# Kernel optimization log

Measured on AMD Instinct MI355X. Metric: run time of the kernel, lower is better.

The kernel has to match this reference:

```python
import jax, jax.numpy as jnp
import numpy as np

N = 30000        # nodes
E = 480000       # edges
IN = 256         # input feature dim
D = 32           # num_hidden per head
H = 4            # heads for layers 0,1
C = 47           # num_classes (final layer, 1 head)
NEG_SLOPE = 0.2


def setup_inputs() -> dict:
    key = jax.random.key(0)
    ks = jax.random.split(key, 16)
    def glorot(k, shape):
        fan = sum(shape)
        return jax.random.normal(k, shape, jnp.float32) * jnp.sqrt(2.0 / fan)
    inp = {
        "x": jax.random.normal(ks[0], (N, IN), jnp.float32),
        # layer 0: IN -> H*D, no residual
        "W0": glorot(ks[1], (IN, H * D)),
        "al0": glorot(ks[2], (H, D)),
        "ar0": glorot(ks[3], (H, D)),
        # layer 1: H*D -> H*D, residual fc
        "W1": glorot(ks[4], (H * D, H * D)),
        "resW1": glorot(ks[5], (H * D, H * D)),
        "al1": glorot(ks[6], (H, D)),
        "ar1": glorot(ks[7], (H, D)),
        # final layer: H*D -> 1*C, residual fc
        "W2": glorot(ks[8], (H * D, 1 * C)),
        "resW2": glorot(ks[9], (H * D, 1 * C)),
        "al2": glorot(ks[10], (1, C)),
        "ar2": glorot(ks[11], (1, C)),
        "src": jax.random.randint(ks[12], (E,), 0, N, jnp.int32),
        "dst": jax.random.randint(ks[13], (E,), 0, N, jnp.int32),
    }
    return inp


def gat_layer(h, W, al, ar, src, dst, heads, d, resW=None, act=None):
    # h: [N, F_in]; W: [F_in, heads*d]; al/ar: [heads, d]
    n = h.shape[0]
    feat = (h @ W).reshape(n, heads, d)                 # [N, H, D]
    el = (feat * al).sum(-1)                            # [N, H]
    er = (feat * ar).sum(-1)                            # [N, H]
    e = jax.nn.leaky_relu(el[src] + er[dst], NEG_SLOPE)  # [E, H]
    # edge softmax over incoming edges of each dst node (numerically stable)
    emax = jax.ops.segment_max(e, dst, num_segments=n)  # [N, H]
    emax = jnp.where(jnp.isfinite(emax), emax, 0.0)     # guard empty segments
    w = jnp.exp(e - emax[dst])                          # [E, H]
    wsum = jax.ops.segment_sum(w, dst, num_segments=n)  # [N, H]
    a = w / jnp.maximum(wsum[dst], 1e-9)                # [E, H]
    msg = feat[src] * a[:, :, None]                     # [E, H, D]
    rst = jax.ops.segment_sum(msg, dst, num_segments=n)  # [N, H, D]
    if resW is not None:
        rst = rst + (h @ resW).reshape(n, heads, d)
    if act is not None:
        rst = act(rst)
    return rst, e


def reference(x, W0, al0, ar0, W1, resW1, al1, ar1, W2, resW2, al2, ar2, src, dst):
    act = jax.nn.elu
    # layer 0 (no residual, no in-conv activation), then flatten + activation
    h, e0 = gat_layer(x, W0, al0, ar0, src, dst, H, D)
    h = act(h.reshape(N, H * D))
    # layer 1 (residual, in-conv activation), then flatten + activation
    h, e1 = gat_layer(h, W1, al1, ar1, src, dst, H, D, resW=resW1, act=act)
    h = act(h.reshape(N, H * D))
    # final layer (residual, no activation), mean over heads
    h, e2 = gat_layer(h, W2, al2, ar2, src, dst, 1, C, resW=resW2)
    logits = h.mean(axis=1)                             # [N, C]
    return (logits, e0, e1, e2)
```

## Files before the change

kernel.cpp:

```cpp
#include <hip/hip_runtime.h>
#include <hip/hip_bf16.h>
#include <math.h>

#define NN 30000
#define NE 480000
#define FIN 256
#define DH 32
#define NH 4
#define NC 47
#define NODE_BLKS 7500
#define EDGE_BLKS 1875
#define SCAN_CHUNK 1024
#define NCHUNKS 30

typedef __attribute__((ext_vector_type(8))) short frag_ab;
typedef __attribute__((ext_vector_type(4))) float f32x4;
typedef __hip_bfloat16 bf16;

static inline size_t align256(size_t x) { return (x + 255) & ~(size_t)255; }

__device__ __forceinline__ short f2bf(float f) {
    union { float f; unsigned u; } c; c.f = f;
    unsigned r = (c.u + 0x7FFFu + ((c.u >> 16) & 1u)) >> 16;
    return (short)r;
}
__device__ __forceinline__ float b2f(unsigned short u) {
    union { unsigned u; float f; } c; c.u = (unsigned)u << 16; return c.f;
}
__device__ __forceinline__ float expw(float v) {
    return __expf((v >= 0.f) ? v : 0.2f * v);
}
__device__ __forceinline__ float lrelu(float v) {
    return (v >= 0.f) ? v : 0.2f * v;
}

__global__ void prep_count(const float* __restrict__ W0, const float* __restrict__ W1,
                           const float* __restrict__ rW1, const float* __restrict__ W2,
                           const float* __restrict__ rW2,
                           const float* __restrict__ al0, const float* __restrict__ ar0,
                           const float* __restrict__ al1, const float* __restrict__ ar1,
                           const float* __restrict__ al2, const float* __restrict__ ar2,
                           bf16* __restrict__ W0t, bf16* __restrict__ W1t,
                           bf16* __restrict__ rW1t, bf16* __restrict__ W2t,
                           bf16* __restrict__ rW2t,
                           const int* __restrict__ dst, int* __restrict__ cnt,
                           int* __restrict__ rank) {
    if (blockIdx.y == 5) {
        int e = blockIdx.x * 256 + threadIdx.x;
        if (e < NE) rank[e] = atomicAdd(&cnt[dst[e]], 1);
        return;
    }
    const float *W, *al, *ar; bf16* Wt; int K, M, rows, H, D;
    switch (blockIdx.y) {
        case 0: W = W0;  Wt = W0t;  K = 256; M = 128; rows = 144; H = 4; D = 32; al = al0; ar = ar0; break;
        case 1: W = W1;  Wt = W1t;  K = 128; M = 128; rows = 144; H = 4; D = 32; al = al1; ar = ar1; break;
        case 2: W = rW1; Wt = rW1t; K = 128; M = 128; rows = 128; H = 0; D = 0;  al = nullptr; ar = nullptr; break;
        case 3: W = W2;  Wt = W2t;  K = 128; M = 47;  rows = 64;  H = 1; D = 47; al = al2; ar = ar2; break;
        default: W = rW2; Wt = rW2t; K = 128; M = 47; rows = 48;  H = 0; D = 0;  al = nullptr; ar = nullptr; break;
    }
    int i = blockIdx.x * 256 + threadIdx.x;
    if (i >= rows * K) return;
    int row = i / K, k = i - row * K;
    float v = 0.f;
    if (row < M) {
        v = W[(long)k * M + row];
    } else if (H > 0 && row < M + 2 * H) {
        int idx = row - M;
        int h = (idx < H) ? idx : idx - H;
        const float* a = (idx < H) ? al : ar;
        float s = 0.f;
        for (int d = 0; d < D; ++d) s += W[(long)k * M + h * D + d] * a[h * D + d];
        v = s;
    }
    Wt[i] = __float2bfloat16(v);
}

__global__ void fill_k(const int* __restrict__ dst, const int* __restrict__ src,
                       const int* __restrict__ rank, const int* __restrict__ loff,
                       const int* __restrict__ bases, int* __restrict__ srcs) {
    int e = blockIdx.x * blockDim.x + threadIdx.x;
    if (e < NE) {
        const int d = dst[e];
        srcs[loff[d] + bases[d >> 10] + rank[e]] = src[e];
    }
}

template <bool A_F32, int NT1, int NT2, int HH, int TAIL>
__global__ __launch_bounds__(256) void gemm_mfma(
    const void* __restrict__ Av, const bf16* __restrict__ B1t,
    const bf16* __restrict__ B2t,
    bf16* __restrict__ C1b, float* __restrict__ el, float* __restrict__ er,
    bf16* __restrict__ C2, int N, int K, int M, int nGemmBlocks,
    const int* __restrict__ t_cnt, int* __restrict__ t_loff, int* __restrict__ t_bsum,
    int* __restrict__ t_bases, int* __restrict__ t_done,
    const float4* __restrict__ pel, const float4* __restrict__ per,
    const int* __restrict__ src, const int* __restrict__ dst,
    float* __restrict__ eout) {
    constexpr int LP = 56;
    __shared__ bf16 As[64][LP];
    __shared__ bf16 Bs1[NT1 * 16][LP];
    __shared__ bf16 Bs2[(NT2 > 0) ? NT2 * 16 : 1][LP];
    __shared__ int ws4[4];

    const int tid = threadIdx.x;

    if constexpr (TAIL == 1) {
        if (blockIdx.x >= nGemmBlocks) {
            const int chunk = blockIdx.x - nGemmBlocks;
            const int lane = tid & 63;
            const int wid = tid >> 6;
            const int g = chunk * SCAN_CHUNK + tid * 4;
            const int a0 = (g + 0 < NN) ? t_cnt[g + 0] : 0;
            const int a1 = (g + 1 < NN) ? t_cnt[g + 1] : 0;
            const int a2 = (g + 2 < NN) ? t_cnt[g + 2] : 0;
            const int a3 = (g + 3 < NN) ? t_cnt[g + 3] : 0;
            const int lsum = a0 + a1 + a2 + a3;
            int x = lsum;
            #pragma unroll
            for (int off = 1; off < 64; off <<= 1) {
                int y = __shfl_up(x, off);
                if (lane >= off) x += y;
            }
            if (lane == 63) ws4[wid] = x;
            __syncthreads();
            int wbase = 0;
            #pragma unroll
            for (int j = 0; j < 4; ++j) if (j < wid) wbase += ws4[j];
            const int excl = wbase + x - lsum;
            if (g + 0 < NN) t_loff[g + 0] = excl;
            if (g + 1 < NN) t_loff[g + 1] = excl + a0;
            if (g + 2 < NN) t_loff[g + 2] = excl + a0 + a1;
            if (g + 3 < NN) t_loff[g + 3] = excl + a0 + a1 + a2;
            if (tid == 0) {
                t_bsum[chunk] = ws4[0] + ws4[1] + ws4[2] + ws4[3];
                __threadfence();
                const int prev = atomicAdd(t_done, 1);
                if (prev == NCHUNKS - 1) {
                    __threadfence();
                    int acc = 0;
                    for (int j = 0; j < NCHUNKS; ++j) { t_bases[j] = acc; acc += t_bsum[j]; }
                    t_bases[NCHUNKS] = acc;
                }
            }
            return;
        }
    }
    if constexpr (TAIL == 2) {
        if (blockIdx.x >= nGemmBlocks) {
            const int e = (blockIdx.x - nGemmBlocks) * 256 + tid;
            const int s = src[e], d = dst[e];
            const float4 a = pel[s], b = per[d];
            float4 v;
            v.x = lrelu(a.x + b.x); v.y = lrelu(a.y + b.y);
            v.z = lrelu(a.z + b.z); v.w = lrelu(a.w + b.w);
            *reinterpret_cast<float4*>(eout + e * 4) = v;
            return;
        }
    }

    const int lane = tid & 63;
    const int wid = tid >> 6;
    const int row0 = blockIdx.x * 64;
    const int l15 = lane & 15;
    const int kq = lane >> 4;

    f32x4 acc1[NT1], acc2[(NT2 > 0) ? NT2 : 1];
    #pragma unroll
    for (int t = 0; t < NT1; ++t) acc1[t] = (f32x4){0.f, 0.f, 0.f, 0.f};
    if constexpr (NT2 > 0) {
        #pragma unroll
        for (int t = 0; t < NT2; ++t) acc2[t] = (f32x4){0.f, 0.f, 0.f, 0.f};
    }

    for (int k0 = 0; k0 < K; k0 += 32) {
        {
            const int r = tid >> 2, kk = (tid & 3) * 8;
            const int gr = row0 + r;
            if constexpr (A_F32) {
                const float* A = (const float*)Av;
                short tmp[8];
                if (gr < N) {
                    const float4 v0 = *(const float4*)&A[(long)gr * K + k0 + kk];
                    const float4 v1 = *(const float4*)&A[(long)gr * K + k0 + kk + 4];
                    tmp[0] = f2bf(v0.x); tmp[1] = f2bf(v0.y); tmp[2] = f2bf(v0.z); tmp[3] = f2bf(v0.w);
                    tmp[4] = f2bf(v1.x); tmp[5] = f2bf(v1.y); tmp[6] = f2bf(v1.z); tmp[7] = f2bf(v1.w);
                } else {
                    #pragma unroll
                    for (int j = 0; j < 8; ++j) tmp[j] = 0;
                }
                *(frag_ab*)&As[r][kk] = *(const frag_ab*)tmp;
            } else {
                const bf16* A = (const bf16*)Av;
                frag_ab v = {0, 0, 0, 0, 0, 0, 0, 0};
                if (gr < N) v = *(const frag_ab*)&A[(long)gr * K + k0 + kk];
                *(frag_ab*)&As[r][kk] = v;
            }
        }
        for (int i = tid; i < NT1 * 64; i += 256) {
            const int c = i >> 2, kk = (i & 3) * 8;
            *(frag_ab*)&Bs1[c][kk] = *(const frag_ab*)&B1t[(long)c * K + k0 + kk];
        }
        if constexpr (NT2 > 0) {
            for (int i = tid; i < NT2 * 64; i += 256) {
                const int c = i >> 2, kk = (i & 3) * 8;
                *(frag_ab*)&Bs2[c][kk] = *(const frag_ab*)&B2t[(long)c * K + k0 + kk];
            }
        }
        __syncthreads();

        const frag_ab a = *(const frag_ab*)&As[wid * 16 + l15][kq * 8];
        #pragma unroll
        for (int t = 0; t < NT1; ++t) {
            const frag_ab b = *(const frag_ab*)&Bs1[t * 16 + l15][kq * 8];
            acc1[t] = __builtin_amdgcn_mfma_f32_16x16x32_bf16(a, b, acc1[t], 0, 0, 0);
        }
        if constexpr (NT2 > 0) {
            #pragma unroll
            for (int t = 0; t < NT2; ++t) {
                const frag_ab b = *(const frag_ab*)&Bs2[t * 16 + l15][kq * 8];
                acc2[t] = __builtin_amdgcn_mfma_f32_16x16x32_bf16(a, b, acc2[t], 0, 0, 0);
            }
        }
        __syncthreads();
    }

    const int r0 = row0 + wid * 16 + kq * 4;
    #pragma unroll
    for (int t = 0; t < NT1; ++t) {
        const int c = t * 16 + l15;
        #pragma unroll
        for (int reg = 0; reg < 4; ++reg) {
            const int r = r0 + reg;
            if (r >= N) continue;
            const float v = acc1[t][reg];
            if (c < M) {
                C1b[(long)r * M + c] = __float2bfloat16(v);
            } else if (c < M + HH) {
                el[(long)r * HH + (c - M)] = v;
            } else if (c < M + 2 * HH) {
                er[(long)r * HH + (c - M - HH)] = v;
            }
        }
    }
    if constexpr (NT2 > 0) {
        #pragma unroll
        for (int t = 0; t < NT2; ++t) {
            const int c = t * 16 + l15;
            if (c >= M) continue;
            #pragma unroll
            for (int reg = 0; reg < 4; ++reg) {
                const int r = r0 + reg;
                if (r < N) C2[(long)r * M + c] = __float2bfloat16(acc2[t][reg]);
            }
        }
    }
}

template <int NELU, bool HAS_RES>
__global__ __launch_bounds__(256) void node_agg4(
    const bf16* __restrict__ featb, const float* __restrict__ el,
    const float4* __restrict__ er4,
    const int* __restrict__ loff, const int* __restrict__ bases,
    const int* __restrict__ srcs,
    const bf16* __restrict__ res, bf16* __restrict__ out) {
    const int node = (int)((blockIdx.x * blockDim.x + threadIdx.x) >> 6);
    const int lane = threadIdx.x & 63;
    const int beg = loff[node] + bases[node >> 10];
    const int end = (node == NN - 1) ? NE : loff[node + 1] + bases[(node + 1) >> 10];

    const int q = lane >> 4;
    const int l15 = lane & 15;
    const int fi = l15 * 8;
    const int h = l15 >> 2;
    const float4 ern4 = er4[node];
    const float ern = (h == 0) ? ern4.x : (h == 1) ? ern4.y : (h == 2) ? ern4.z : ern4.w;

    float a[8] = {0.f, 0.f, 0.f, 0.f, 0.f, 0.f, 0.f, 0.f};
    float sl = 0.f;
    int i = beg + q;
    for (; i + 4 < end; i += 8) {
        const int iB = i + 4;
        const int snA = srcs[i], snB = srcs[iB];
        const float wA = expw(el[snA * 4 + h] + ern);
        const float wB = expw(el[snB * 4 + h] + ern);
        sl += wA + wB;
        const frag_ab fA = *(const frag_ab*)(featb + (long)snA * 128 + fi);
        const frag_ab fB = *(const frag_ab*)(featb + (long)snB * 128 + fi);
        #pragma unroll
        for (int j = 0; j < 8; ++j)
            a[j] += wA * b2f((unsigned short)fA[j]) + wB * b2f((unsigned short)fB[j]);
    }
    for (; i < end; i += 4) {
        const int sn = srcs[i];
        const float w = expw(el[sn * 4 + h] + ern);
        sl += w;
        const frag_ab f = *(const frag_ab*)(featb + (long)sn * 128 + fi);
        #pragma unroll
        for (int j = 0; j < 8; ++j) a[j] += w * b2f((unsigned short)f[j]);
    }
    sl += __shfl_xor(sl, 16);
    sl += __shfl_xor(sl, 32);
    #pragma unroll
    for (int j = 0; j < 8; ++j) {
        a[j] += __shfl_xor(a[j], 16);
        a[j] += __shfl_xor(a[j], 32);
    }

    if (lane < 16) {
        const float inv = 1.f / fmaxf(sl, 1e-9f);
        float v[8];
        #pragma unroll
        for (int j = 0; j < 8; ++j) v[j] = a[j] * inv;
        if constexpr (HAS_RES) {
            const frag_ab rr = *(const frag_ab*)(res + (long)node * 128 + fi);
            #pragma unroll
            for (int j = 0; j < 8; ++j) v[j] += b2f((unsigned short)rr[j]);
        }
        #pragma unroll
        for (int t = 0; t < NELU; ++t)
            #pragma unroll
            for (int j = 0; j < 8; ++j)
                v[j] = (v[j] > 0.f) ? v[j] : expm1f(v[j]);
        frag_ab o;
        #pragma unroll
        for (int j = 0; j < 8; ++j) o[j] = f2bf(v[j]);
        *(frag_ab*)(out + (long)node * 128 + fi) = o;
    }
}

__global__ __launch_bounds__(256) void final_k(
    const bf16* __restrict__ featb, const float* __restrict__ el2s,
    const float* __restrict__ er2s, float* __restrict__ es1,
    const int* __restrict__ loff, const int* __restrict__ bases,
    const int* __restrict__ srcs,
    const bf16* __restrict__ res, float* __restrict__ logits,
    const int* __restrict__ src, const int* __restrict__ dst,
    float* __restrict__ e2) {
    __shared__ float sc1[4][64];
    if (blockIdx.x < NODE_BLKS) {
        const int node = (int)((blockIdx.x * blockDim.x + threadIdx.x) >> 6);
        const int lane = threadIdx.x & 63;
        const int wid = threadIdx.x >> 6;
        const int beg = loff[node] + bases[node >> 10];
        const int end = (node == NN - 1) ? NE : loff[node + 1] + bases[(node + 1) >> 10];
        const float ern = er2s[node];

        float s = 0.f;
        for (int i = beg + lane; i < end; i += 64) {
            const float t = expw(el2s[srcs[i]] + ern);
            s += t;
            const int idx = i - beg;
            if (idx < 64) sc1[wid][idx] = t;
            else es1[i] = t;
        }
        #pragma unroll
        for (int off = 32; off > 0; off >>= 1) s += __shfl_xor(s, off);
        const float inv = 1.f / fmaxf(s, 1e-9f);
        __syncthreads();

        const bool active = lane < NC;
        float acc = 0.f;
        int i = beg;
        for (; i + 8 <= end; i += 8) {
            const int d0 = i - beg;
            int sn[8]; float w[8];
            #pragma unroll
            for (int k = 0; k < 8; ++k) {
                sn[k] = srcs[i + k];
                w[k] = (d0 + k < 64) ? sc1[wid][d0 + k] : es1[i + k];
            }
            if (active) {
                #pragma unroll
                for (int k = 0; k < 8; ++k)
                    acc += w[k] * __bfloat162float(featb[(long)sn[k] * NC + lane]);
            }
        }
        for (; i < end; ++i) {
            const int idx = i - beg;
            const float w = (idx < 64) ? sc1[wid][idx] : es1[i];
            if (active) acc += w * __bfloat162float(featb[(long)srcs[i] * NC + lane]);
        }
        if (active) {
            logits[(long)node * NC + lane] =
                acc * inv + __bfloat162float(res[(long)node * NC + lane]);
        }
    } else {
        const int e = (blockIdx.x - NODE_BLKS) * 256 + threadIdx.x;
        e2[e] = lrelu(el2s[src[e]] + er2s[dst[e]]);
    }
}

extern "C" void kernel_launch(void* const* d_in, const int* in_sizes, int n_in,
                              void* d_out, int out_size, void* d_ws, size_t ws_size,
                              hipStream_t stream) {
    const float* x     = (const float*)d_in[0];
    const float* W0    = (const float*)d_in[1];
    const float* al0   = (const float*)d_in[2];
    const float* ar0   = (const float*)d_in[3];
    const float* W1    = (const float*)d_in[4];
    const float* resW1 = (const float*)d_in[5];
    const float* al1   = (const float*)d_in[6];
    const float* ar1   = (const float*)d_in[7];
    const float* W2    = (const float*)d_in[8];
    const float* resW2 = (const float*)d_in[9];
    const float* al2   = (const float*)d_in[10];
    const float* ar2   = (const float*)d_in[11];
    const int*   src   = (const int*)d_in[12];
    const int*   dst   = (const int*)d_in[13];

    float* out    = (float*)d_out;
    float* logits = out;
    float* e0     = out + (long)NN * NC;
    float* e1     = e0 + (long)NE * NH;
    float* e2     = e1 + (long)NE * NH;

    char* p = (char*)d_ws;
    int* cnt    = (int*)p; p += align256(sizeof(int) * (NN + 64));
    int* done   = cnt + NN;
    int* loff   = (int*)p; p += align256(sizeof(int) * (NN + 1));
    int* bsum   = (int*)p; p += align256(sizeof(int) * 32);
    int* bases  = (int*)p; p += align256(sizeof(int) * 32);
    int* rank   = (int*)p; p += align256(sizeof(int) * NE);
    int* srcs   = (int*)p; p += align256(sizeof(int) * NE);
    float* el0b = (float*)p; p += align256(sizeof(float) * NN * NH);
    float* er0b = (float*)p; p += align256(sizeof(float) * NN * NH);
    float* el1b = (float*)p; p += align256(sizeof(float) * NN * NH);
    float* er1b = (float*)p; p += align256(sizeof(float) * NN * NH);
    float* el2b = (float*)p; p += align256(sizeof(float) * NN);
    float* er2b = (float*)p; p += align256(sizeof(float) * NN);
    float* es   = (float*)p; p += align256(sizeof(float) * NE);
    bf16* resb  = (bf16*)p; p += align256(sizeof(bf16) * (long)NN * 128);
    bf16* featb = (bf16*)p; p += align256(sizeof(bf16) * (long)NN * 128);
    bf16* hb    = (bf16*)p; p += align256(sizeof(bf16) * (long)NN * 128);
    bf16* W0t   = (bf16*)p; p += align256(sizeof(bf16) * 144 * 256);
    bf16* W1t   = (bf16*)p; p += align256(sizeof(bf16) * 144 * 128);
    bf16* rW1t  = (bf16*)p; p += align256(sizeof(bf16) * 128 * 128);
    bf16* W2t   = (bf16*)p; p += align256(sizeof(bf16) * 64 * 128);
    bf16* rW2t  = (bf16*)p; p += align256(sizeof(bf16) * 48 * 128);

    const int gemmBlocks = (NN + 63) / 64;

    hipMemsetAsync(cnt, 0, sizeof(int) * (NN + 64), stream);
    prep_count<<<dim3(EDGE_BLKS, 6), 256, 0, stream>>>(
        W0, W1, resW1, W2, resW2, al0, ar0, al1, ar1, al2, ar2,
        W0t, W1t, rW1t, W2t, rW2t, dst, cnt, rank);

    gemm_mfma<true, 9, 0, NH, 1><<<gemmBlocks + NCHUNKS, 256, 0, stream>>>(
        x, W0t, nullptr, featb, el0b, er0b, nullptr, NN, FIN, 128, gemmBlocks,
        cnt, loff, bsum, bases, done, nullptr, nullptr, nullptr, nullptr, nullptr);

    fill_k<<<EDGE_BLKS, 256, 0, stream>>>(dst, src, rank, loff, bases, srcs);

    node_agg4<1, false><<<NODE_BLKS, 256, 0, stream>>>(
        featb, el0b, (const float4*)er0b, loff, bases, srcs, nullptr, hb);

    gemm_mfma<false, 9, 8, NH, 2><<<gemmBlocks + EDGE_BLKS, 256, 0, stream>>>(
        hb, W1t, rW1t, featb, el1b, er1b, resb, NN, 128, 128, gemmBlocks,
        nullptr, nullptr, nullptr, nullptr, nullptr,
        (const float4*)el0b, (const float4*)er0b, src, dst, e0);

    node_agg4<2, true><<<NODE_BLKS, 256, 0, stream>>>(
        featb, el1b, (const float4*)er1b, loff, bases, srcs, resb, hb);

    gemm_mfma<false, 4, 3, 1, 2><<<gemmBlocks + EDGE_BLKS, 256, 0, stream>>>(
        hb, W2t, rW2t, featb, el2b, er2b, resb, NN, 128, NC, gemmBlocks,
        nullptr, nullptr, nullptr, nullptr, nullptr,
        (const float4*)el1b, (const float4*)er1b, src, dst, e1);

    final_k<<<NODE_BLKS + EDGE_BLKS, 256, 0, stream>>>(
        featb, el2b, er2b, es, loff, bases, srcs, resb, logits, src, dst, e2);
}
```

Baseline: 178.0 us.

## Pad final-layer features to 48 and fuse softmax into single-pass aggregation

The final-layer weights are padded so feat and residual rows have a stride of 48 instead of 47. That allows aligned 2-element bf16 loads, with each half-wavefront handling alternate edges. The final kernel now computes the edge exponentials and the weighted feature sum in one pass, normalising at the end. This removes the shared-memory and global scratch spill of exp weights and the block barrier. In exchange, every active lane recomputes the exp per edge, and the change depends on the GEMM honouring the new output width of 48.

```diff
diff --git a/kernel.cpp b/kernel.cpp
--- a/kernel.cpp
+++ b/kernel.cpp
@@ -50,26 +50,26 @@
         if (e < NE) rank[e] = atomicAdd(&cnt[dst[e]], 1);
         return;
     }
-    const float *W, *al, *ar; bf16* Wt; int K, M, rows, H, D;
+    const float *W, *al, *ar; bf16* Wt; int K, Msrc, Mpad, rows, H, D;
     switch (blockIdx.y) {
-        case 0: W = W0;  Wt = W0t;  K = 256; M = 128; rows = 144; H = 4; D = 32; al = al0; ar = ar0; break;
-        case 1: W = W1;  Wt = W1t;  K = 128; M = 128; rows = 144; H = 4; D = 32; al = al1; ar = ar1; break;
-        case 2: W = rW1; Wt = rW1t; K = 128; M = 128; rows = 128; H = 0; D = 0;  al = nullptr; ar = nullptr; break;
-        case 3: W = W2;  Wt = W2t;  K = 128; M = 47;  rows = 64;  H = 1; D = 47; al = al2; ar = ar2; break;
-        default: W = rW2; Wt = rW2t; K = 128; M = 47; rows = 48;  H = 0; D = 0;  al = nullptr; ar = nullptr; break;
+        case 0: W = W0;  Wt = W0t;  K = 256; Msrc = 128; Mpad = 128; rows = 144; H = 4; D = 32; al = al0; ar = ar0; break;
+        case 1: W = W1;  Wt = W1t;  K = 128; Msrc = 128; Mpad = 128; rows = 144; H = 4; D = 32; al = al1; ar = ar1; break;
+        case 2: W = rW1; Wt = rW1t; K = 128; Msrc = 128; Mpad = 128; rows = 128; H = 0; D = 0;  al = nullptr; ar = nullptr; break;
+        case 3: W = W2;  Wt = W2t;  K = 128; Msrc = 47;  Mpad = 48;  rows = 64;  H = 1; D = 47; al = al2; ar = ar2; break;
+        default: W = rW2; Wt = rW2t; K = 128; Msrc = 47; Mpad = 48;  rows = 48;  H = 0; D = 0;  al = nullptr; ar = nullptr; break;
     }
     int i = blockIdx.x * 256 + threadIdx.x;
     if (i >= rows * K) return;
     int row = i / K, k = i - row * K;
     float v = 0.f;
-    if (row < M) {
-        v = W[(long)k * M + row];
-    } else if (H > 0 && row < M + 2 * H) {
-        int idx = row - M;
+    if (row < Msrc) {
+        v = W[(long)k * Msrc + row];
+    } else if (H > 0 && row >= Mpad && row < Mpad + 2 * H) {
+        int idx = row - Mpad;
         int h = (idx < H) ? idx : idx - H;
         const float* a = (idx < H) ? al : ar;
         float s = 0.f;
-        for (int d = 0; d < D; ++d) s += W[(long)k * M + h * D + d] * a[h * D + d];
+        for (int d = 0; d < D; ++d) s += W[(long)k * Msrc + h * D + d] * a[h * D + d];
         v = s;
     }
     Wt[i] = __float2bfloat16(v);
@@ -329,60 +329,61 @@
 }
 
 __global__ __launch_bounds__(256) void final_k(
-    const bf16* __restrict__ featb, const float* __restrict__ el2s,
-    const float* __restrict__ er2s, float* __restrict__ es1,
+    const bf16* __restrict__ featb48, const float* __restrict__ el2s,
+    const float* __restrict__ er2s,
     const int* __restrict__ loff, const int* __restrict__ bases,
     const int* __restrict__ srcs,
-    const bf16* __restrict__ res, float* __restrict__ logits,
+    const bf16* __restrict__ res48, float* __restrict__ logits,
     const int* __restrict__ src, const int* __restrict__ dst,
     float* __restrict__ e2) {
-    __shared__ float sc1[4][64];
     if (blockIdx.x < NODE_BLKS) {
         const int node = (int)((blockIdx.x * blockDim.x + threadIdx.x) >> 6);
         const int lane = threadIdx.x & 63;
-        const int wid = threadIdx.x >> 6;
         const int beg = loff[node] + bases[node >> 10];
         const int end = (node == NN - 1) ? NE : loff[node + 1] + bases[(node + 1) >> 10];
         const float ern = er2s[node];
 
-        float s = 0.f;
-        for (int i = beg + lane; i < end; i += 64) {
-            const float t = expw(el2s[srcs[i]] + ern);
-            s += t;
-            const int idx = i - beg;
-            if (idx < 64) sc1[wid][idx] = t;
-            else es1[i] = t;
-        }
-        #pragma unroll
-        for (int off = 32; off > 0; off >>= 1) s += __shfl_xor(s, off);
-        const float inv = 1.f / fmaxf(s, 1e-9f);
-        __syncthreads();
-
-        const bool active = lane < NC;
-        float acc = 0.f;
-        int i = beg;
-        for (; i + 8 <= end; i += 8) {
-            const int d0 = i - beg;
-            int sn[8]; float w[8];
-            #pragma unroll
-            for (int k = 0; k < 8; ++k) {
-                sn[k] = srcs[i + k];
-                w[k] = (d0 + k < 64) ? sc1[wid][d0 + k] : es1[i + k];
-            }
-            if (active) {
-                #pragma unroll
-                for (int k = 0; k < 8; ++k)
-                    acc += w[k] * __bfloat162float(featb[(long)sn[k] * NC + lane]);
-            }
-        }
-        for (; i < end; ++i) {
-            const int idx = i - beg;
-            const float w = (idx < 64) ? sc1[wid][idx] : es1[i];
-            if (active) acc += w * __bfloat162float(featb[(long)srcs[i] * NC + lane]);
-        }
-        if (active) {
-            logits[(long)node * NC + lane] =
-                acc * inv + __bfloat162float(res[(long)node * NC + lane]);
+        const int half = lane >> 5;
+        const int l31 = lane & 31;
+        const bool act = l31 < 24;
+        const int fi = l31 * 2;
+
+        float a0 = 0.f, a1 = 0.f, sl = 0.f;
+        int i = beg + half;
+        for (; i + 2 < end; i += 4) {
+            const int iB = i + 2;
+            const int snA = srcs[i], snB = srcs[iB];
+            const float wA = expw(el2s[snA] + ern);
+            const float wB = expw(el2s[snB] + ern);
+            sl += wA + wB;
+            if (act) {
+                const ushort2 fA = *(const ushort2*)(featb48 + (long)snA * 48 + fi);
+                const ushort2 fB = *(const ushort2*)(featb48 + (long)snB * 48 + fi);
+                a0 += wA * b2f(fA.x) + wB * b2f(fB.x);
+                a1 += wA * b2f(fA.y) + wB * b2f(fB.y);
+            }
+        }
+        for (; i < end; i += 2) {
+            const int sn = srcs[i];
+            const float w = expw(el2s[sn] + ern);
+            sl += w;
+            if (act) {
+                const ushort2 f = *(const ushort2*)(featb48 + (long)sn * 48 + fi);
+                a0 += w * b2f(f.x);
+                a1 += w * b2f(f.y);
+            }
+        }
+        const float s = __shfl(sl, 0) + __shfl(sl, 32);
+        a0 += __shfl_xor(a0, 32);
+        a1 += __shfl_xor(a1, 32);
+
+        if (lane < 24) {
+            const float inv = 1.f / fmaxf(s, 1e-9f);
+            const ushort2 rr = *(const ushort2*)(res48 + (long)node * 48 + fi);
+            const float v0 = a0 * inv + b2f(rr.x);
+            const float v1 = a1 * inv + b2f(rr.y);
+            logits[(long)node * NC + fi] = v0;
+            if (fi + 1 < NC) logits[(long)node * NC + fi + 1] = v1;
         }
     } else {
         const int e = (blockIdx.x - NODE_BLKS) * 256 + threadIdx.x;
@@ -428,7 +429,6 @@
     float* er1b = (float*)p; p += align256(sizeof(float) * NN * NH);
     float* el2b = (float*)p; p += align256(sizeof(float) * NN);
     float* er2b = (float*)p; p += align256(sizeof(float) * NN);
-    float* es   = (float*)p; p += align256(sizeof(float) * NE);
     bf16* resb  = (bf16*)p; p += align256(sizeof(bf16) * (long)NN * 128);
     bf16* featb = (bf16*)p; p += align256(sizeof(bf16) * (long)NN * 128);
     bf16* hb    = (bf16*)p; p += align256(sizeof(bf16) * (long)NN * 128);
@@ -463,10 +463,10 @@
         featb, el1b, (const float4*)er1b, loff, bases, srcs, resb, hb);
 
     gemm_mfma<false, 4, 3, 1, 2><<<gemmBlocks + EDGE_BLKS, 256, 0, stream>>>(
-        hb, W2t, rW2t, featb, el2b, er2b, resb, NN, 128, NC, gemmBlocks,
+        hb, W2t, rW2t, featb, el2b, er2b, resb, NN, 128, 48, gemmBlocks,
         nullptr, nullptr, nullptr, nullptr, nullptr,
         (const float4*)el1b, (const float4*)er1b, src, dst, e1);
 
     final_k<<<NODE_BLKS + EDGE_BLKS, 256, 0, stream>>>(
-        featb, el2b, er2b, es, loff, bases, srcs, resb, logits, src, dst, e2);
-}
+        featb, el2b, er2b, loff, bases, srcs, resb, logits, src, dst, e2);
+}
```

Measured after the change: 176.1 us, median of 2. No clear change (-1.1%).
